# Optimization experiments

Hardware: AMD Instinct MI355X
Metric: run time of the kernel (lower is better)

The kernel has to match this reference:

```python
import jax, jax.numpy as jnp
import numpy as np
import math

B, N, DMODEL, H = 8, 1024, 256, 8
HEAD_DIM = DMODEL // H


def setup_inputs() -> dict:
    key = jax.random.key(0)
    ks = jax.random.split(key, 8)
    x = jax.random.normal(ks[0], (B, N, DMODEL), dtype=jnp.float32)
    # symmetric-ish nonnegative pairwise distances
    adj = jax.random.uniform(ks[1], (B, N, N), dtype=jnp.float32) * 10.0
    mask = jax.random.uniform(ks[2], (B, N)) < 0.9  # bool, mostly valid nodes
    W_qkv = jax.random.normal(ks[3], (DMODEL, 3 * DMODEL), dtype=jnp.float32) / math.sqrt(DMODEL)
    b_qkv = jax.random.normal(ks[4], (3 * DMODEL,), dtype=jnp.float32) * 0.01
    shifts = jnp.arange(1.0, H + 1.0, dtype=jnp.float32)  # initial_shifts
    widths = jnp.ones((H,), dtype=jnp.float32)            # initial_widths
    # self_loop_W = 1/head_dim + U(0,1), non-trainable
    self_loop_w = 1.0 / HEAD_DIM + jax.random.uniform(ks[5], (H,), dtype=jnp.float32)
    return {"x": x, "adj": adj, "mask": mask, "W_qkv": W_qkv, "b_qkv": b_qkv,
            "shifts": shifts, "widths": widths, "self_loop_w": self_loop_w}


def reference(x, adj, mask, W_qkv, b_qkv, shifts, widths, self_loop_w):
    b, n, _ = x.shape
    h = shifts.shape[0]
    d = W_qkv.shape[1] // (3 * h)
    qkv = (x @ W_qkv + b_qkv).reshape(b, n, 3, h, d)
    qkv = jnp.transpose(qkv, (2, 0, 3, 1, 4))  # [3, B, H, N, D]
    Q, K, V = qkv[0], qkv[1], qkv[2]
    scores = jnp.einsum('bhnd,bhmd->bhnm', Q, K) / jnp.sqrt(jnp.float32(d))
    # Gaussian moire focus on adjacency distances, per head
    sh = shifts.reshape(1, h, 1, 1)
    w = jnp.maximum(widths, 0.5).reshape(1, h, 1, 1)
    moire = jnp.exp(-((adj[:, None, :, :] - sh) ** 2) / w)
    adjusted = scores + jnp.log(jnp.maximum(moire, 1e-6))
    eye = jnp.eye(n, dtype=adjusted.dtype)  # [N, N]
    adjusted = adjusted + eye * self_loop_w.reshape(1, h, 1, 1)
    mask2d = (mask[:, :, None] & mask[:, None, :])[:, None, :, :]  # [B,1,N,N]
    adjusted = jnp.where(mask2d, adjusted, jnp.float32(-1000000.0))
    attn = jax.nn.softmax(adjusted, axis=-1)
    out = jnp.einsum('bhnm,bhmd->bhnd', attn, V)
    return jnp.transpose(out, (0, 2, 1, 3)).reshape(b, n, h * d)
```

## Files before the change

### kernel.cpp

```cpp
#include <hip/hip_runtime.h>

#define BB 8
#define NN 1024
#define DM 256
#define HH 8
#define HD 32
#define TC 768

typedef __bf16 bf16x8 __attribute__((ext_vector_type(8)));
typedef __bf16 bf16x4 __attribute__((ext_vector_type(4)));
typedef float  f32x4  __attribute__((ext_vector_type(4)));

__global__ __launch_bounds__(256) void precast(
    const float* __restrict__ x, const float* __restrict__ W,
    __bf16* __restrict__ xb, __bf16* __restrict__ Wt)
{
  const int tid = threadIdx.x;
  const int bid = blockIdx.x;
  if (bid < 48) {
    __shared__ __bf16 T[64][65];
    const int ct = bid % 12, kt = bid / 12;
    const int c0 = ct * 64, k0 = kt * 64;
    #pragma unroll
    for (int i = 0; i < 16; ++i) {
      int e = tid + i * 256, kk = e >> 6, cc = e & 63;
      T[cc][kk] = (__bf16)W[(size_t)(k0 + kk) * TC + c0 + cc];
    }
    __syncthreads();
    #pragma unroll
    for (int i = 0; i < 16; ++i) {
      int e = tid + i * 256, cc = e >> 6, kk = e & 63;
      Wt[(size_t)(c0 + cc) * DM + k0 + kk] = T[cc][kk];
    }
  } else {
    const size_t e = (size_t)(bid - 48) * 256 + tid;
    const float4 v = ((const float4*)x)[e];
    bf16x4 o;
    o[0] = (__bf16)v.x; o[1] = (__bf16)v.y;
    o[2] = (__bf16)v.z; o[3] = (__bf16)v.w;
    ((bf16x4*)xb)[e] = o;
  }
}

__global__ __launch_bounds__(256, 4) void qkv_gemm(
    const __bf16* __restrict__ xb, const __bf16* __restrict__ Wt,
    const float* __restrict__ bias, __bf16* __restrict__ Qb,
    __bf16* __restrict__ Kb, __bf16* __restrict__ Vt)
{
  __shared__ __align__(16) char U[18432];
  __bf16* As = (__bf16*)U;
  __bf16* Bs = (__bf16*)(U + 10240);

  const int tid  = threadIdx.x;
  const int w    = tid >> 6, lane = tid & 63;
  const int n16  = lane & 15, quad = lane >> 4;
  const int m0   = blockIdx.y * 128, c0 = blockIdx.x * 64;
  const int bb   = m0 >> 10, n0 = m0 & 1023;

  const int arow = tid >> 1, ahalf = tid & 1;
  const int bc   = tid & 63, bkh = tid >> 6;

  f32x4 acc[2][4] = {};

  const __bf16* xa_base = &xb[(size_t)(m0 + arow) * DM + ahalf * 16];
  const __bf16* wb_base = &Wt[(size_t)(c0 + bc) * DM + bkh * 8];
  bf16x8 ra0 = *(const bf16x8*)&xa_base[0];
  bf16x8 ra1 = *(const bf16x8*)&xa_base[8];
  bf16x8 rb  = *(const bf16x8*)&wb_base[0];

  for (int k0 = 0; k0 < DM; k0 += 32) {
    *(bf16x8*)&As[arow*40 + ahalf*16]     = ra0;
    *(bf16x8*)&As[arow*40 + ahalf*16 + 8] = ra1;
    *(bf16x8*)&Bs[bc*40 + bkh*8]          = rb;
    __syncthreads();
    if (k0 + 32 < DM) {
      ra0 = *(const bf16x8*)&xa_base[k0 + 32];
      ra1 = *(const bf16x8*)&xa_base[k0 + 40];
      rb  = *(const bf16x8*)&wb_base[k0 + 32];
    }
    bf16x8 af0 = *(const bf16x8*)&As[(w*32 + n16)*40 + quad*8];
    bf16x8 af1 = *(const bf16x8*)&As[(w*32 + 16 + n16)*40 + quad*8];
    #pragma unroll
    for (int cb = 0; cb < 4; ++cb) {
      bf16x8 bf = *(const bf16x8*)&Bs[(cb*16 + n16)*40 + quad*8];
      acc[0][cb] = __builtin_amdgcn_mfma_f32_16x16x32_bf16(af0, bf, acc[0][cb], 0, 0, 0);
      acc[1][cb] = __builtin_amdgcn_mfma_f32_16x16x32_bf16(af1, bf, acc[1][cb], 0, 0, 0);
    }
    __syncthreads();
  }

  float bv[4];
  #pragma unroll
  for (int cb = 0; cb < 4; ++cb) bv[cb] = bias[c0 + cb*16 + n16];

  if (c0 < 512) {
    __bf16* Ct = (__bf16*)U;
    #pragma unroll
    for (int cb = 0; cb < 4; ++cb)
      #pragma unroll
      for (int mb = 0; mb < 2; ++mb)
        #pragma unroll
        for (int r = 0; r < 4; ++r)
          Ct[(w*32 + mb*16 + quad*4 + r)*72 + cb*16 + n16] =
              (__bf16)(acc[mb][cb][r] + bv[cb]);
    __syncthreads();
    const int chunk = tid & 3, hh = (tid >> 2) & 1, rbase = tid >> 3;
    const int c_head = c0 + hh*32;
    const int h = (c_head >> 5) & 7;
    __bf16* base = (c_head >> 8) ? Kb : Qb;
    #pragma unroll
    for (int it = 0; it < 4; ++it) {
      int rl = rbase + it*32;
      bf16x8 v = *(const bf16x8*)&Ct[rl*72 + hh*32 + chunk*8];
      *(bf16x8*)&base[((size_t)((bb*HH + h)*NN + n0 + rl))*HD + chunk*8] = v;
    }
  } else {
    __bf16* CtT = (__bf16*)U;
    #pragma unroll
    for (int cb = 0; cb < 4; ++cb)
      #pragma unroll
      for (int mb = 0; mb < 2; ++mb) {
        bf16x4 t;
        #pragma unroll
        for (int r = 0; r < 4; ++r) t[r] = (__bf16)(acc[mb][cb][r] + bv[cb]);
        *(bf16x4*)&CtT[(cb*16 + n16)*136 + w*32 + mb*16 + quad*4] = t;
      }
    __syncthreads();
    const int col = tid >> 2, sg = tid & 3;
    const int c = c0 + col;
    const int h = (c >> 5) & 7, dd = c & 31;
    __bf16* dst = &Vt[((size_t)((bb*HH + h)*HD + dd))*NN + n0 + sg*32];
    const __bf16* srcp = &CtT[col*136 + sg*32];
    #pragma unroll
    for (int q2 = 0; q2 < 4; ++q2)
      *(bf16x8*)&dst[q2*8] = *(const bf16x8*)&srcp[q2*8];
  }
}

__global__ __launch_bounds__(256, 4) void attn_kernel(
    const __bf16* __restrict__ Q, const __bf16* __restrict__ K,
    const __bf16* __restrict__ Vt, const float* __restrict__ adj,
    const int* __restrict__ mask, const float* __restrict__ shifts,
    const float* __restrict__ widths, const float* __restrict__ slw,
    float* __restrict__ out)
{
  __shared__ __align__(16) char U[9216];
  __bf16 (*Ps)[72] = (__bf16(*)[72])U;
  __shared__ __align__(16) __bf16 Ks[2][64][40];
  __shared__ __align__(16) __bf16 Vts[2][32][72];

  const int tid  = threadIdx.x;
  const int w    = tid >> 6, lane = tid & 63;
  const int n16  = lane & 15, quad = lane >> 4;
  const int bh   = blockIdx.x >> 4, qt = blockIdx.x & 15;
  const int b    = bh >> 3, h = bh & 7;
  const int q0   = qt * 64;

  const float L2E   = 1.4426950408889634f;
  const float sh    = shifts[h];
  const float ninvw = -L2E / fmaxf(widths[h], 0.5f);
  const float slv   = slw[h] * L2E;
  const float scl   = 0.17677669529663687f * L2E;
  const float MASKV = -28.0f;
  const float c1 = -2.0f * sh * ninvw;
  const float c2 = sh * sh * ninvw;

  const int srow = tid >> 2, sseg = tid & 3;
  const int vd   = tid >> 3, vsg  = tid & 7;

  const __bf16* Kg = K + (size_t)bh*NN*HD;
  const __bf16* Vg = Vt + (size_t)bh*HD*NN;

  const bf16x8 qf =
      *(const bf16x8*)&Q[((size_t)bh*NN + q0 + w*16 + n16)*HD + quad*8];

  {
    *(bf16x8*)&Ks[0][srow][sseg*8] = *(const bf16x8*)&Kg[srow*HD + sseg*8];
    *(bf16x8*)&Vts[0][vd][vsg*8]   = *(const bf16x8*)&Vg[(size_t)vd*NN + vsg*8];
  }
  int mq[4];
  #pragma unroll
  for (int r = 0; r < 4; ++r) mq[r] = mask[b*NN + q0 + w*16 + quad*4 + r];

  const float* arow0 = adj + ((size_t)(b*NN + q0 + w*16 + quad*4))*NN + n16;
  const float* arow1 = arow0 + NN;
  const float* arow2 = arow0 + 2*NN;
  const float* arow3 = arow0 + 3*NN;
  const int*   mrp   = mask + b*NN + n16;

  float av[2][4][4];
  int   mj[2][4];
  #pragma unroll
  for (int cb = 0; cb < 4; ++cb) mj[0][cb] = mrp[cb*16];
  #pragma unroll
  for (int cb = 0; cb < 4; ++cb) {
    av[0][0][cb] = arow0[cb*16];
    av[0][1][cb] = arow1[cb*16];
    av[0][2][cb] = arow2[cb*16];
    av[0][3][cb] = arow3[cb*16];
  }
  arow0 += 64; arow1 += 64; arow2 += 64; arow3 += 64; mrp += 64;

  const f32x4 zero = {0.f, 0.f, 0.f, 0.f};
  f32x4 o0 = zero, o1 = zero, lacc = zero;
  bf16x8 onesb;
  #pragma unroll
  for (int i = 0; i < 8; ++i) onesb[i] = (__bf16)1.0f;

  const int sa = (n16 & 12) << 1;

  __syncthreads();

  #pragma unroll 2
  for (int jtl = 0; jtl < 16; ++jtl) {
    const int cur = jtl & 1, nxt = cur ^ 1;
    const int j0  = jtl * 64;

    bf16x8 kn, vn;
    if (jtl < 15) {
      kn = *(const bf16x8*)&Kg[(j0 + 64 + srow)*HD + sseg*8];
      vn = *(const bf16x8*)&Vg[(size_t)vd*NN + j0 + 64 + vsg*8];
      #pragma unroll
      for (int cb = 0; cb < 4; ++cb) mj[nxt][cb] = mrp[cb*16];
      #pragma unroll
      for (int cb = 0; cb < 4; ++cb) {
        av[nxt][0][cb] = arow0[cb*16];
        av[nxt][1][cb] = arow1[cb*16];
        av[nxt][2][cb] = arow2[cb*16];
        av[nxt][3][cb] = arow3[cb*16];
      }
      arow0 += 64; arow1 += 64; arow2 += 64; arow3 += 64; mrp += 64;
    }

    f32x4 s[4];
    #pragma unroll
    for (int cb = 0; cb < 4; ++cb) {
      bf16x8 kf = *(const bf16x8*)&Ks[cur][cb*16 + n16][quad*8];
      s[cb] = __builtin_amdgcn_mfma_f32_16x16x32_bf16(qf, kf, zero, 0, 0, 0);
    }

    const bool diagtile = (jtl == qt);
    #pragma unroll
    for (int r = 0; r < 4; ++r) {
      const int rowl = w*16 + quad*4 + r;
      #pragma unroll
      for (int cb = 0; cb < 4; ++cb) {
        float a   = av[cur][r][cb];
        float mo  = fmaf(a, fmaf(a, ninvw, c1), c2);
        float val = fmaf(s[cb][r], scl, mo);
        if (diagtile && (cb*16 + n16 == rowl)) val += slv;
        bool ok = (mq[r] != 0) && (mj[cur][cb] != 0);
        val = ok ? val : MASKV;
        float p = __builtin_amdgcn_exp2f(val);
        Ps[rowl][(cb*16 + n16) ^ (quad*8)] = (__bf16)p;
      }
    }

    bf16x8 a0  = *(const bf16x8*)&Ps[w*16 + n16][(quad*8) ^ sa];
    bf16x8 a1  = *(const bf16x8*)&Ps[w*16 + n16][32 + ((quad*8) ^ sa)];
    bf16x8 b00 = *(const bf16x8*)&Vts[cur][n16][quad*8];
    bf16x8 b01 = *(const bf16x8*)&Vts[cur][n16][32 + quad*8];
    bf16x8 b10 = *(const bf16x8*)&Vts[cur][16 + n16][quad*8];
    bf16x8 b11 = *(const bf16x8*)&Vts[cur][16 + n16][32 + quad*8];
    o0   = __builtin_amdgcn_mfma_f32_16x16x32_bf16(a0, b00, o0, 0, 0, 0);
    o0   = __builtin_amdgcn_mfma_f32_16x16x32_bf16(a1, b01, o0, 0, 0, 0);
    o1   = __builtin_amdgcn_mfma_f32_16x16x32_bf16(a0, b10, o1, 0, 0, 0);
    o1   = __builtin_amdgcn_mfma_f32_16x16x32_bf16(a1, b11, o1, 0, 0, 0);
    lacc = __builtin_amdgcn_mfma_f32_16x16x32_bf16(a0, onesb, lacc, 0, 0, 0);
    lacc = __builtin_amdgcn_mfma_f32_16x16x32_bf16(a1, onesb, lacc, 0, 0, 0);

    if (jtl < 15) {
      *(bf16x8*)&Ks[nxt][srow][sseg*8] = kn;
      *(bf16x8*)&Vts[nxt][vd][vsg*8]   = vn;
    }
    __syncthreads();
  }

  #pragma unroll
  for (int r = 0; r < 4; ++r) {
    const float invl = 1.0f / lacc[r];
    const int n = q0 + w*16 + quad*4 + r;
    float* og = out + ((size_t)(b*NN + n))*DM + h*HD;
    og[n16]      = o0[r] * invl;
    og[16 + n16] = o1[r] * invl;
  }
}

extern "C" void kernel_launch(void* const* d_in, const int* in_sizes, int n_in,
                              void* d_out, int out_size, void* d_ws, size_t ws_size,
                              hipStream_t stream) {
  const float* x      = (const float*)d_in[0];
  const float* adj    = (const float*)d_in[1];
  const int*   mask   = (const int*)d_in[2];
  const float* W      = (const float*)d_in[3];
  const float* bias   = (const float*)d_in[4];
  const float* shifts = (const float*)d_in[5];
  const float* widths = (const float*)d_in[6];
  const float* slwp   = (const float*)d_in[7];
  float* out = (float*)d_out;

  const size_t BHND = (size_t)BB*HH*NN*HD;
  const size_t WTN  = (size_t)TC*DM;
  __bf16* xbuf = (__bf16*)d_ws;
  __bf16* Wt   = xbuf + BHND;
  __bf16* Qb   = Wt + WTN;
  __bf16* Kb   = Qb + BHND;
  __bf16* Vt   = Kb + BHND;

  precast<<<dim3(48 + (int)(BHND/4/256)), 256, 0, stream>>>(x, W, xbuf, Wt);
  qkv_gemm<<<dim3(TC/64, (BB*NN)/128), 256, 0, stream>>>(xbuf, Wt, bias, Qb, Kb, Vt);
  attn_kernel<<<dim3(BB*HH*16), 256, 0, stream>>>(Qb, Kb, Vt, adj, mask,
                                                  shifts, widths, slwp, out);
}
```

Before: 140.3 us.

## Use direct global-to-LDS loads in QKV GEMM and transpose score layout in attention

The QKV GEMM now stages 64-wide K slices straight from global memory into swizzled, double-buffered LDS with global_load_lds, replacing the register-staged 32-wide loop. In the attention kernel the score MFMA operands are swapped so each lane holds four consecutive key columns of one query row. That lets the adjacency and mask be read as 16-byte vectors instead of scalar strided loads, and P is written to a swizzled LDS tile as packed bf16 pairs. The GEMM's LDS footprint grows to 48KB and its occupancy hint drops from 4 to 3, which could limit latency hiding.

```diff
diff --git a/kernel.cpp b/kernel.cpp
--- a/kernel.cpp
+++ b/kernel.cpp
@@ -9,7 +9,10 @@
 
 typedef __bf16 bf16x8 __attribute__((ext_vector_type(8)));
 typedef __bf16 bf16x4 __attribute__((ext_vector_type(4)));
+typedef __bf16 bf16x2 __attribute__((ext_vector_type(2)));
 typedef float  f32x4  __attribute__((ext_vector_type(4)));
+typedef int    i32x4  __attribute__((ext_vector_type(4)));
+typedef unsigned int u32;
 
 __global__ __launch_bounds__(256) void precast(
     const float* __restrict__ x, const float* __restrict__ W,
@@ -42,14 +45,16 @@
   }
 }
 
-__global__ __launch_bounds__(256, 4) void qkv_gemm(
+__global__ __launch_bounds__(256, 3) void qkv_gemm(
     const __bf16* __restrict__ xb, const __bf16* __restrict__ Wt,
     const float* __restrict__ bias, __bf16* __restrict__ Qb,
     __bf16* __restrict__ Kb, __bf16* __restrict__ Vt)
 {
-  __shared__ __align__(16) char U[18432];
-  __bf16* As = (__bf16*)U;
-  __bf16* Bs = (__bf16*)(U + 10240);
+  __shared__ __align__(16) char LDSU[49152];
+  __bf16* As0 = (__bf16*)LDSU;
+  __bf16* Bs0 = (__bf16*)(LDSU + 16384);
+  __bf16* As1 = (__bf16*)(LDSU + 24576);
+  __bf16* Bs1 = (__bf16*)(LDSU + 40960);
 
   const int tid  = threadIdx.x;
   const int w    = tid >> 6, lane = tid & 63;
@@ -57,34 +62,53 @@
   const int m0   = blockIdx.y * 128, c0 = blockIdx.x * 64;
   const int bb   = m0 >> 10, n0 = m0 & 1023;
 
-  const int arow = tid >> 1, ahalf = tid & 1;
-  const int bc   = tid & 63, bkh = tid >> 6;
+  const int stRow = w*8 + (lane >> 3);
+  const int stG   = (lane & 7) ^ (lane >> 3);
+  const __bf16* gA = &xb[(size_t)(m0 + stRow)*DM + stG*8];
+  const __bf16* gB = &Wt[(size_t)(c0 + stRow)*DM + stG*8];
+
+#define QKV_STAGE(Adst, Bdst, K0) do {                                        \
+    _Pragma("unroll")                                                         \
+    for (int i_ = 0; i_ < 4; ++i_) {                                          \
+      const __bf16* gp_ = gA + (size_t)(i_*32)*DM + (K0);                     \
+      __bf16* lp_ = (Adst) + (i_*32 + w*8)*64;                                \
+      __builtin_amdgcn_global_load_lds(                                       \
+          (const __attribute__((address_space(1))) u32*)gp_,                  \
+          (__attribute__((address_space(3))) u32*)lp_, 16, 0, 0);             \
+    }                                                                         \
+    _Pragma("unroll")                                                         \
+    for (int i_ = 0; i_ < 2; ++i_) {                                          \
+      const __bf16* gp_ = gB + (size_t)(i_*32)*DM + (K0);                     \
+      __bf16* lp_ = (Bdst) + (i_*32 + w*8)*64;                                \
+      __builtin_amdgcn_global_load_lds(                                       \
+          (const __attribute__((address_space(1))) u32*)gp_,                  \
+          (__attribute__((address_space(3))) u32*)lp_, 16, 0, 0);             \
+    }                                                                         \
+  } while (0)
 
   f32x4 acc[2][4] = {};
 
-  const __bf16* xa_base = &xb[(size_t)(m0 + arow) * DM + ahalf * 16];
-  const __bf16* wb_base = &Wt[(size_t)(c0 + bc) * DM + bkh * 8];
-  bf16x8 ra0 = *(const bf16x8*)&xa_base[0];
-  bf16x8 ra1 = *(const bf16x8*)&xa_base[8];
-  bf16x8 rb  = *(const bf16x8*)&wb_base[0];
-
-  for (int k0 = 0; k0 < DM; k0 += 32) {
-    *(bf16x8*)&As[arow*40 + ahalf*16]     = ra0;
-    *(bf16x8*)&As[arow*40 + ahalf*16 + 8] = ra1;
-    *(bf16x8*)&Bs[bc*40 + bkh*8]          = rb;
-    __syncthreads();
-    if (k0 + 32 < DM) {
-      ra0 = *(const bf16x8*)&xa_base[k0 + 32];
-      ra1 = *(const bf16x8*)&xa_base[k0 + 40];
-      rb  = *(const bf16x8*)&wb_base[k0 + 32];
-    }
-    bf16x8 af0 = *(const bf16x8*)&As[(w*32 + n16)*40 + quad*8];
-    bf16x8 af1 = *(const bf16x8*)&As[(w*32 + 16 + n16)*40 + quad*8];
-    #pragma unroll
-    for (int cb = 0; cb < 4; ++cb) {
-      bf16x8 bf = *(const bf16x8*)&Bs[(cb*16 + n16)*40 + quad*8];
-      acc[0][cb] = __builtin_amdgcn_mfma_f32_16x16x32_bf16(af0, bf, acc[0][cb], 0, 0, 0);
-      acc[1][cb] = __builtin_amdgcn_mfma_f32_16x16x32_bf16(af1, bf, acc[1][cb], 0, 0, 0);
+  QKV_STAGE(As0, Bs0, 0);
+  __syncthreads();
+
+  #pragma unroll
+  for (int kk = 0; kk < 4; ++kk) {
+    __bf16* Ac = (kk & 1) ? As1 : As0;
+    __bf16* Bc = (kk & 1) ? Bs1 : Bs0;
+    if (kk == 0)      QKV_STAGE(As1, Bs1, 64);
+    else if (kk == 1) QKV_STAGE(As0, Bs0, 128);
+    else if (kk == 2) QKV_STAGE(As1, Bs1, 192);
+    #pragma unroll
+    for (int ks = 0; ks < 2; ++ks) {
+      const int ch = ((ks*4 + quad) ^ (n16 & 7)) * 8;
+      bf16x8 af0 = *(const bf16x8*)&Ac[(w*32 + n16)*64 + ch];
+      bf16x8 af1 = *(const bf16x8*)&Ac[(w*32 + 16 + n16)*64 + ch];
+      #pragma unroll
+      for (int cb = 0; cb < 4; ++cb) {
+        bf16x8 bfb = *(const bf16x8*)&Bc[(cb*16 + n16)*64 + ch];
+        acc[0][cb] = __builtin_amdgcn_mfma_f32_16x16x32_bf16(af0, bfb, acc[0][cb], 0, 0, 0);
+        acc[1][cb] = __builtin_amdgcn_mfma_f32_16x16x32_bf16(af1, bfb, acc[1][cb], 0, 0, 0);
+      }
     }
     __syncthreads();
   }
@@ -94,7 +118,7 @@
   for (int cb = 0; cb < 4; ++cb) bv[cb] = bias[c0 + cb*16 + n16];
 
   if (c0 < 512) {
-    __bf16* Ct = (__bf16*)U;
+    __bf16* Ct = (__bf16*)LDSU;
     #pragma unroll
     for (int cb = 0; cb < 4; ++cb)
       #pragma unroll
@@ -115,7 +139,7 @@
       *(bf16x8*)&base[((size_t)((bb*HH + h)*NN + n0 + rl))*HD + chunk*8] = v;
     }
   } else {
-    __bf16* CtT = (__bf16*)U;
+    __bf16* CtT = (__bf16*)LDSU;
     #pragma unroll
     for (int cb = 0; cb < 4; ++cb)
       #pragma unroll
@@ -144,8 +168,7 @@
     const float* __restrict__ widths, const float* __restrict__ slw,
     float* __restrict__ out)
 {
-  __shared__ __align__(16) char U[9216];
-  __bf16 (*Ps)[72] = (__bf16(*)[72])U;
+  __shared__ __align__(16) char PsU[8192];
   __shared__ __align__(16) __bf16 Ks[2][64][40];
   __shared__ __align__(16) __bf16 Vts[2][32][72];
 
@@ -178,36 +201,28 @@
     *(bf16x8*)&Ks[0][srow][sseg*8] = *(const bf16x8*)&Kg[srow*HD + sseg*8];
     *(bf16x8*)&Vts[0][vd][vsg*8]   = *(const bf16x8*)&Vg[(size_t)vd*NN + vsg*8];
   }
-  int mq[4];
-  #pragma unroll
-  for (int r = 0; r < 4; ++r) mq[r] = mask[b*NN + q0 + w*16 + quad*4 + r];
-
-  const float* arow0 = adj + ((size_t)(b*NN + q0 + w*16 + quad*4))*NN + n16;
-  const float* arow1 = arow0 + NN;
-  const float* arow2 = arow0 + 2*NN;
-  const float* arow3 = arow0 + 3*NN;
-  const int*   mrp   = mask + b*NN + n16;
-
-  float av[2][4][4];
-  int   mj[2][4];
-  #pragma unroll
-  for (int cb = 0; cb < 4; ++cb) mj[0][cb] = mrp[cb*16];
-  #pragma unroll
-  for (int cb = 0; cb < 4; ++cb) {
-    av[0][0][cb] = arow0[cb*16];
-    av[0][1][cb] = arow1[cb*16];
-    av[0][2][cb] = arow2[cb*16];
-    av[0][3][cb] = arow3[cb*16];
-  }
-  arow0 += 64; arow1 += 64; arow2 += 64; arow3 += 64; mrp += 64;
+
+  const bool mqv = mask[b*NN + q0 + w*16 + n16] != 0;
+
+  const float* aq  = adj + ((size_t)(b*NN + q0 + w*16 + n16))*NN + quad*4;
+  const int*   mjp = mask + b*NN + quad*4;
+
+  f32x4 av[2][4];
+  #pragma unroll
+  for (int cb = 0; cb < 4; ++cb) av[0][cb] = *(const f32x4*)&aq[cb*16];
+
+  char* PsRow = PsU + (w*16 + n16)*128;
+  const int swzM  = (n16 & 7) * 16;
+  const int swzW  = (quad*8) ^ swzM;
+  const int swzR0 = (quad*16) ^ swzM;
+  const int swzR1 = (64 + quad*16) ^ swzM;
+  const int dloc  = w*16 + n16 - quad*4;
 
   const f32x4 zero = {0.f, 0.f, 0.f, 0.f};
   f32x4 o0 = zero, o1 = zero, lacc = zero;
   bf16x8 onesb;
   #pragma unroll
   for (int i = 0; i < 8; ++i) onesb[i] = (__bf16)1.0f;
-
-  const int sa = (n16 & 12) << 1;
 
   __syncthreads();
 
@@ -221,43 +236,44 @@
       kn = *(const bf16x8*)&Kg[(j0 + 64 + srow)*HD + sseg*8];
       vn = *(const bf16x8*)&Vg[(size_t)vd*NN + j0 + 64 + vsg*8];
       #pragma unroll
-      for (int cb = 0; cb < 4; ++cb) mj[nxt][cb] = mrp[cb*16];
-      #pragma unroll
-      for (int cb = 0; cb < 4; ++cb) {
-        av[nxt][0][cb] = arow0[cb*16];
-        av[nxt][1][cb] = arow1[cb*16];
-        av[nxt][2][cb] = arow2[cb*16];
-        av[nxt][3][cb] = arow3[cb*16];
-      }
-      arow0 += 64; arow1 += 64; arow2 += 64; arow3 += 64; mrp += 64;
-    }
+      for (int cb = 0; cb < 4; ++cb)
+        av[nxt][cb] = *(const f32x4*)&aq[j0 + 64 + cb*16];
+    }
+
+    i32x4 mj[4];
+    #pragma unroll
+    for (int cb = 0; cb < 4; ++cb) mj[cb] = *(const i32x4*)&mjp[j0 + cb*16];
 
     f32x4 s[4];
     #pragma unroll
     for (int cb = 0; cb < 4; ++cb) {
       bf16x8 kf = *(const bf16x8*)&Ks[cur][cb*16 + n16][quad*8];
-      s[cb] = __builtin_amdgcn_mfma_f32_16x16x32_bf16(qf, kf, zero, 0, 0, 0);
+      s[cb] = __builtin_amdgcn_mfma_f32_16x16x32_bf16(kf, qf, zero, 0, 0, 0);
     }
 
     const bool diagtile = (jtl == qt);
     #pragma unroll
-    for (int r = 0; r < 4; ++r) {
-      const int rowl = w*16 + quad*4 + r;
-      #pragma unroll
-      for (int cb = 0; cb < 4; ++cb) {
-        float a   = av[cur][r][cb];
+    for (int cb = 0; cb < 4; ++cb) {
+      float p[4];
+      #pragma unroll
+      for (int r = 0; r < 4; ++r) {
+        float a   = av[cur][cb][r];
         float mo  = fmaf(a, fmaf(a, ninvw, c1), c2);
         float val = fmaf(s[cb][r], scl, mo);
-        if (diagtile && (cb*16 + n16 == rowl)) val += slv;
-        bool ok = (mq[r] != 0) && (mj[cur][cb] != 0);
+        if (diagtile && (cb*16 + r == dloc)) val += slv;
+        bool ok = mqv && (mj[cb][r] != 0);
         val = ok ? val : MASKV;
-        float p = __builtin_amdgcn_exp2f(val);
-        Ps[rowl][(cb*16 + n16) ^ (quad*8)] = (__bf16)p;
+        p[r] = __builtin_amdgcn_exp2f(val);
       }
-    }
-
-    bf16x8 a0  = *(const bf16x8*)&Ps[w*16 + n16][(quad*8) ^ sa];
-    bf16x8 a1  = *(const bf16x8*)&Ps[w*16 + n16][32 + ((quad*8) ^ sa)];
+      bf16x2 w0, w1;
+      w0[0] = (__bf16)p[0]; w0[1] = (__bf16)p[1];
+      w1[0] = (__bf16)p[2]; w1[1] = (__bf16)p[3];
+      *(bf16x2*)(PsRow + ((cb*32 + 0) ^ swzW)) = w0;
+      *(bf16x2*)(PsRow + ((cb*32 + 4) ^ swzW)) = w1;
+    }
+
+    bf16x8 a0  = *(const bf16x8*)(PsRow + swzR0);
+    bf16x8 a1  = *(const bf16x8*)(PsRow + swzR1);
     bf16x8 b00 = *(const bf16x8*)&Vts[cur][n16][quad*8];
     bf16x8 b01 = *(const bf16x8*)&Vts[cur][n16][32 + quad*8];
     bf16x8 b10 = *(const bf16x8*)&Vts[cur][16 + n16][quad*8];
```

After: 147.5 us. 1.05x slower.
